# Performance work log

Measured on AMD Instinct MI355X. Metric: run time of the kernel, lower is better.

## Reference

```python
import jax, jax.numpy as jnp
import numpy as np

N_NODES = 100000
SIG_DIM = 64
N_ADJ = 1600000
N_QUERY = 262144


def setup_inputs() -> dict:
    key = jax.random.key(0)
    k1, k2, k3, k4, k5 = jax.random.split(key, 5)
    x = jax.random.normal(k1, (N_NODES, SIG_DIM), dtype=jnp.float32)
    x = x / jnp.linalg.norm(x, axis=1, keepdims=True)  # F.normalize(p=2, dim=1)
    node_weight = jax.random.uniform(k2, (N_NODES,), dtype=jnp.float32)
    edges = jax.random.randint(k3, (2, N_QUERY), 0, N_NODES)
    adj_row = jnp.sort(jax.random.randint(k4, (N_ADJ,), 0, N_NODES))
    adj_col = jax.random.randint(k5, (N_ADJ,), 0, N_NODES)
    return {
        "x": x,
        "node_weight": node_weight,
        "edges": edges,
        "adj_row": adj_row,
        "adj_col": adj_col,
        "num_nodes": N_NODES,
    }


def reference(x, node_weight, edges, adj_row, adj_col, num_nodes):
    # node signatures scaled by node weight
    xw = x * node_weight[:, None]                      # [N, D]

    seg = lambda vals: jax.ops.segment_sum(vals, adj_row, num_segments=num_nodes)

    # SpMM propagation: (A @ x)[i] = sum_{j in N(i)} x[j]
    one_hop = seg(xw[adj_col])                          # [N, D]
    deg = seg(jnp.ones_like(adj_row, dtype=xw.dtype))   # [N]
    two_iter = seg(one_hop[adj_col])                    # [N, D]

    # combine mode
    two_hop = two_iter - one_hop - xw
    deg2 = jnp.maximum(seg(deg[adj_col]) - deg - 1.0, 0.0)

    row, col = edges[0], edges[1]
    x_u_1 = one_hop[row]
    x_v_1 = one_hop[col]
    x_u_2 = two_hop[row]
    x_v_2 = two_hop[col]

    dot = lambda a, b: (a * b).sum(axis=-1)

    deg_u = deg[row]
    deg_v = deg[col]
    deg_u_2 = deg2[row]
    deg_v_2 = deg2[col]

    count_1_1 = dot(x_u_1, x_v_1)
    count_1_2 = dot(x_u_1, x_v_2)
    count_2_1 = dot(x_u_2, x_v_1)
    count_2_2 = dot(x_u_2, x_v_2)
    count_1_inf = deg_u + deg_v - 2 * count_1_1 - count_1_2 - count_2_1
    count_2_inf = deg_u_2 + deg_v_2 - 2 * count_2_2 - count_1_2 - count_2_1

    x_u_iter = two_iter[row]
    x_v_iter = two_iter[col]
    x_u = xw[row]
    x_v = xw[col]
    comb_count_1_2 = dot(x_u_1, x_v_iter)
    comb_count_2_1 = dot(x_u_iter, x_v_1)
    comb_count_2_2 = dot(x_u_iter - deg_u[:, None] * x_u,
                         x_v_iter - deg_v[:, None] * x_v)
    comb_count_self_1_2 = dot(x_u_1, x_u_iter)
    comb_count_self_2_1 = dot(x_v_1, x_v_iter)

    features = jnp.stack([
        count_1_1, count_1_2, count_2_1, count_2_2,
        count_1_inf, count_2_inf,
        comb_count_1_2, comb_count_2_1, comb_count_2_2,
        comb_count_self_1_2, comb_count_self_2_1,
        deg_u, deg_v, deg_u_2, deg_v_2,
    ], axis=1)                                          # [E, 15]
    return features
```

## Files before the change

kernel.cpp:

```cpp
#include <hip/hip_runtime.h>


#define D 64

typedef unsigned int uint32;
typedef _Float16 h2 __attribute__((ext_vector_type(2)));

union U32H2 { uint32 u; h2 h; };
__device__ __forceinline__ h2 u_as_h2(uint32 u) { U32H2 t; t.u = u; return t.h; }

__device__ __forceinline__ uint32 pack2(float a, float b) {
    uint32 ua = __float_as_uint(a);
    ua += 0x7fffu + ((ua >> 16) & 1u);
    uint32 ub = __float_as_uint(b);
    ub += 0x7fffu + ((ub >> 16) & 1u);
    return (ua >> 16) | (ub & 0xffff0000u);
}
__device__ __forceinline__ float lo2f(uint32 u) { return __uint_as_float(u << 16); }
__device__ __forceinline__ float hi2f(uint32 u) { return __uint_as_float(u & 0xffff0000u); }

__device__ __forceinline__ uint32 enc1(float v) {
    float a = fabsf(v);
    uint32 s = (__float_as_uint(v) >> 24) & 0x80u;
    if (a >= 448.f) return s | 0x7Eu;
    if (a < 0.015625f) {
        uint32 m = (uint32)rintf(a * 512.f);
        return (m > 7u) ? (s | 0x08u) : (s | m);
    }
    uint32 b = __float_as_uint(a);
    b += 0x7FFFFu + ((b >> 20) & 1u);
    uint32 m3 = (b >> 20) & 7u;
    int e4 = (int)(b >> 23) - 127 + 7;
    if (e4 > 15) return s | 0x7Eu;
    return s | ((uint32)e4 << 3) | m3;
}

__device__ __forceinline__ void dec8(uint32 u, uint32& pe, uint32& po) {
    uint32 se = (u << 8) & 0x80008000u;
    uint32 ue = u & 0x007f007fu;
    pe = ((ue << 7) + 0x08000800u) | se;
    uint32 so = u & 0x80008000u;
    uint32 uo = (u >> 8) & 0x007f007fu;
    po = ((uo << 7) + 0x08000800u) | so;
}

#define RED_GRP(v)  { v += __shfl_xor(v, 1, 64); v += __shfl_xor(v, 2, 64);  v += __shfl_xor(v, 4, 64);  }

__global__ void __launch_bounds__(256) prep_kernel(const float4* __restrict__ x,
                                                   const float* __restrict__ w,
                                                   uint2* __restrict__ xw,
                                                   const int* __restrict__ adj_row,
                                                   int* __restrict__ row_ptr,
                                                   int n8, int n, int nadj, int xw_blocks) {
    if ((int)blockIdx.x < xw_blocks) {
        int i = blockIdx.x * blockDim.x + threadIdx.x;
        if (i >= n8) return;
        float s = w[i >> 3] * 64.f;
        float4 a = x[i * 2], b = x[i * 2 + 1];
        uint32 w0 = enc1(a.x * s) | (enc1(a.z * s) << 8)
                  | (enc1(a.y * s) << 16) | (enc1(a.w * s) << 24);
        uint32 w1 = enc1(b.x * s) | (enc1(b.z * s) << 8)
                  | (enc1(b.y * s) << 16) | (enc1(b.w * s) << 24);
        xw[i] = make_uint2(w0, w1);
    } else {
        int i = (blockIdx.x - xw_blocks) * blockDim.x + threadIdx.x;
        if (i > n) return;
        int lo = 0, hi = nadj;
        while (lo < hi) {
            int mid = (lo + hi) >> 1;
            if (adj_row[mid] < i) lo = mid + 1; else hi = mid;
        }
        row_ptr[i] = lo;
    }
}

__global__ void __launch_bounds__(256) spmm1_kernel(const uint2* __restrict__ src,
                                                    const int* __restrict__ row_ptr,
                                                    const int* __restrict__ adj_col,
                                                    uint4* __restrict__ dst,
                                                    float* __restrict__ degout,
                                                    int n) {
    int lane = threadIdx.x & 63;
    int sub = lane & 7;
    int node = blockIdx.x * 32 + (threadIdx.x >> 6) * 8 + (lane >> 3);
    if (node >= n) return;
    int start = row_ptr[node], end = row_ptr[node + 1];
    int deg_n = end - start;
    h2 acc0 = u_as_h2(0u), acc1 = u_as_h2(0u), acc2 = u_as_h2(0u), acc3 = u_as_h2(0u);
    int gbase = lane & 56;
    const int* colp = adj_col + start;
    int base = 0;
    for (; base + 16 <= deg_n; base += 16) {
        int idx0 = colp[base + sub];
        int idx1 = colp[base + 8 + sub];
#pragma unroll
        for (int i = 0; i < 8; ++i) {
            int c0 = __shfl(idx0, gbase + i, 64);
            int c1 = __shfl(idx1, gbase + i, 64);
            uint2 q0 = src[(size_t)c0 * 8 + sub];
            uint2 q1 = src[(size_t)c1 * 8 + sub];
            uint32 pe, po;
            dec8(q0.x, pe, po);
            acc0 += u_as_h2(pe); acc1 += u_as_h2(po);
            dec8(q0.y, pe, po);
            acc2 += u_as_h2(pe); acc3 += u_as_h2(po);
            dec8(q1.x, pe, po);
            acc0 += u_as_h2(pe); acc1 += u_as_h2(po);
            dec8(q1.y, pe, po);
            acc2 += u_as_h2(pe); acc3 += u_as_h2(po);
        }
    }
    for (; base + 8 <= deg_n; base += 8) {
        int idx = colp[base + sub];
#pragma unroll
        for (int i = 0; i < 8; ++i) {
            int c = __shfl(idx, gbase + i, 64);
            uint2 qv = src[(size_t)c * 8 + sub];
            uint32 pe, po;
            dec8(qv.x, pe, po);
            acc0 += u_as_h2(pe); acc1 += u_as_h2(po);
            dec8(qv.y, pe, po);
            acc2 += u_as_h2(pe); acc3 += u_as_h2(po);
        }
    }
    if (base < deg_n) {
        int k = base + sub;
        int idx = (k < deg_n) ? colp[k] : 0;
#pragma unroll
        for (int i = 0; i < 8; ++i) {
            if (base + i < deg_n) {
                int c = __shfl(idx, gbase + i, 64);
                uint2 qv = src[(size_t)c * 8 + sub];
                uint32 pe, po;
                dec8(qv.x, pe, po);
                acc0 += u_as_h2(pe); acc1 += u_as_h2(po);
                dec8(qv.y, pe, po);
                acc2 += u_as_h2(pe); acc3 += u_as_h2(po);
            }
        }
    }
    uint4 o;
    o.x = pack2((float)acc0.x, (float)acc0.y);
    o.y = pack2((float)acc1.x, (float)acc1.y);
    o.z = pack2((float)acc2.x, (float)acc2.y);
    o.w = pack2((float)acc3.x, (float)acc3.y);
    dst[(size_t)node * 8 + sub] = o;
    if (sub == 0) degout[node] = (float)deg_n;
}

__global__ void __launch_bounds__(256) spmm2_kernel(const uint4* __restrict__ src,
                                                    const int* __restrict__ row_ptr,
                                                    const int* __restrict__ adj_col,
                                                    const float* __restrict__ degv,
                                                    uint4* __restrict__ dst,
                                                    float2* __restrict__ degpair,
                                                    int n) {
    int lane = threadIdx.x & 63;
    int sub = lane & 7;
    int node = blockIdx.x * 32 + (threadIdx.x >> 6) * 8 + (lane >> 3);
    if (node >= n) return;
    int start = row_ptr[node], end = row_ptr[node + 1];
    int deg_n = end - start;
    float a0 = 0.f, a1 = 0.f, a2 = 0.f, a3 = 0.f,
          a4 = 0.f, a5 = 0.f, a6 = 0.f, a7 = 0.f;
    float dsum = 0.f;
    int gbase = lane & 56;
    const int* colp = adj_col + start;

#define SPMM2_BLK(IDX)                                                 \
    {                                                                  \
        dsum += degv[IDX];                                             \
        _Pragma("unroll")                                              \
        for (int i = 0; i < 8; ++i) {                                  \
            int c = __shfl(IDX, gbase + i, 64);                        \
            uint4 qv = src[(size_t)c * 8 + sub];                       \
            a0 += lo2f(qv.x); a1 += hi2f(qv.x);                        \
            a2 += lo2f(qv.y); a3 += hi2f(qv.y);                        \
            a4 += lo2f(qv.z); a5 += hi2f(qv.z);                        \
            a6 += lo2f(qv.w); a7 += hi2f(qv.w);                        \
        }                                                              \
    }

    int nfull = deg_n >> 3;
    if (nfull > 0) {
        int idx = colp[sub];
        for (int b = 1; b < nfull; ++b) {
            int idxn = colp[b * 8 + sub];
            SPMM2_BLK(idx)
            idx = idxn;
        }
        SPMM2_BLK(idx)
    }
    int base = nfull * 8;
    if (base < deg_n) {
        int k = base + sub;
        bool kv = k < deg_n;
        int idx = kv ? colp[k] : 0;
        if (kv) dsum += degv[idx];
#pragma unroll
        for (int i = 0; i < 8; ++i) {
            if (base + i < deg_n) {
                int c = __shfl(idx, gbase + i, 64);
                uint4 qv = src[(size_t)c * 8 + sub];
                a0 += lo2f(qv.x); a1 += hi2f(qv.x);
                a2 += lo2f(qv.y); a3 += hi2f(qv.y);
                a4 += lo2f(qv.z); a5 += hi2f(qv.z);
                a6 += lo2f(qv.w); a7 += hi2f(qv.w);
            }
        }
    }
#undef SPMM2_BLK
    uint4 o;
    o.x = pack2(a0, a1); o.y = pack2(a2, a3);
    o.z = pack2(a4, a5); o.w = pack2(a6, a7);
    dst[(size_t)node * 8 + sub] = o;
    RED_GRP(dsum)
    if (sub == 0)
        degpair[node] = make_float2((float)deg_n,
                                    fmaxf(dsum - (float)deg_n - 1.0f, 0.0f));
}

__global__ void __launch_bounds__(256) edge_kernel(const int* __restrict__ edges,
                                                   const uint2* __restrict__ xw,
                                                   const uint4* __restrict__ h1,
                                                   const uint4* __restrict__ t2,
                                                   const float2* __restrict__ degpair,
                                                   float* __restrict__ out,
                                                   int E) {
    __shared__ float so[32 * 15];
    int t = blockIdx.x * blockDim.x + threadIdx.x;
    int q = t >> 3, sub = t & 7;
    bool valid = q < E;
    if (valid) {
        int u = edges[q], v = edges[E + q];
        uint2 pxu = xw[(size_t)u * 8 + sub], pxv = xw[(size_t)v * 8 + sub];
        uint4 phu = h1[(size_t)u * 8 + sub], phv = h1[(size_t)v * 8 + sub];
        uint4 ptu = t2[(size_t)u * 8 + sub], ptv = t2[(size_t)v * 8 + sub];
        float2 dpu = degpair[u], dpv = degpair[v];
        float du = dpu.x, du2 = dpu.y, dv = dpv.x, dv2 = dpv.y;

        float fxu[8], fxv[8], fhu[8], fhv[8], ftu[8], ftv[8];
        {
            uint32 pe, po;
            dec8(pxu.x, pe, po);
            h2 e = u_as_h2(pe), o_ = u_as_h2(po);
            fxu[0] = (float)e.x; fxu[1] = (float)e.y; fxu[2] = (float)o_.x; fxu[3] = (float)o_.y;
            dec8(pxu.y, pe, po);
            e = u_as_h2(pe); o_ = u_as_h2(po);
            fxu[4] = (float)e.x; fxu[5] = (float)e.y; fxu[6] = (float)o_.x; fxu[7] = (float)o_.y;
            dec8(pxv.x, pe, po);
            e = u_as_h2(pe); o_ = u_as_h2(po);
            fxv[0] = (float)e.x; fxv[1] = (float)e.y; fxv[2] = (float)o_.x; fxv[3] = (float)o_.y;
            dec8(pxv.y, pe, po);
            e = u_as_h2(pe); o_ = u_as_h2(po);
            fxv[4] = (float)e.x; fxv[5] = (float)e.y; fxv[6] = (float)o_.x; fxv[7] = (float)o_.y;
        }
        fhu[0]=lo2f(phu.x); fhu[1]=hi2f(phu.x); fhu[2]=lo2f(phu.y); fhu[3]=hi2f(phu.y);
        fhu[4]=lo2f(phu.z); fhu[5]=hi2f(phu.z); fhu[6]=lo2f(phu.w); fhu[7]=hi2f(phu.w);
        fhv[0]=lo2f(phv.x); fhv[1]=hi2f(phv.x); fhv[2]=lo2f(phv.y); fhv[3]=hi2f(phv.y);
        fhv[4]=lo2f(phv.z); fhv[5]=hi2f(phv.z); fhv[6]=lo2f(phv.w); fhv[7]=hi2f(phv.w);
        ftu[0]=lo2f(ptu.x); ftu[1]=hi2f(ptu.x); ftu[2]=lo2f(ptu.y); ftu[3]=hi2f(ptu.y);
        ftu[4]=lo2f(ptu.z); ftu[5]=hi2f(ptu.z); ftu[6]=lo2f(ptu.w); ftu[7]=hi2f(ptu.w);
        ftv[0]=lo2f(ptv.x); ftv[1]=hi2f(ptv.x); ftv[2]=lo2f(ptv.y); ftv[3]=hi2f(ptv.y);
        ftv[4]=lo2f(ptv.z); ftv[5]=hi2f(ptv.z); ftv[6]=lo2f(ptv.w); ftv[7]=hi2f(ptv.w);

        float c11 = 0.f, c12 = 0.f, c21 = 0.f, c22 = 0.f,
              cc12 = 0.f, cc21 = 0.f, cc22 = 0.f, cs12 = 0.f, cs21 = 0.f;
#pragma unroll
        for (int j = 0; j < 8; ++j) {
            float xu = fxu[j], xv = fxv[j];
            float hu = fhu[j], hv = fhv[j];
            float tu = ftu[j], tv = ftv[j];
            float h2u = tu - hu - xu, h2v = tv - hv - xv;
            float au = fmaf(-du, xu, tu), av = fmaf(-dv, xv, tv);
            c11  = fmaf(hu,  hv,  c11);
            c12  = fmaf(hu,  h2v, c12);
            c21  = fmaf(h2u, hv,  c21);
            c22  = fmaf(h2u, h2v, c22);
            cc12 = fmaf(hu,  tv,  cc12);
            cc21 = fmaf(tu,  hv,  cc21);
            cc22 = fmaf(au,  av,  cc22);
            cs12 = fmaf(hu,  tu,  cs12);
            cs21 = fmaf(hv,  tv,  cs21);
        }
        RED_GRP(c11) RED_GRP(c12) RED_GRP(c21) RED_GRP(c22)
        RED_GRP(cc12) RED_GRP(cc21) RED_GRP(cc22) RED_GRP(cs12) RED_GRP(cs21)

        if (sub == 0) {
            float* o = so + (threadIdx.x >> 3) * 15;
            o[0]  = c11;
            o[1]  = c12;
            o[2]  = c21;
            o[3]  = c22;
            o[4]  = du + dv - 2.f * c11 - c12 - c21;
            o[5]  = du2 + dv2 - 2.f * c22 - c12 - c21;
            o[6]  = cc12;
            o[7]  = cc21;
            o[8]  = cc22;
            o[9]  = cs12;
            o[10] = cs21;
            o[11] = du;
            o[12] = dv;
            o[13] = du2;
            o[14] = dv2;
        }
    }
    __syncthreads();
    int eb = blockIdx.x * 32;
    if (eb < E) {
        int nval = E - eb; if (nval > 32) nval = 32;
        int nflt = nval * 15;
        size_t obase = (size_t)eb * 15;
        for (int k = threadIdx.x; k < nflt; k += 256)
            out[obase + k] = so[k];
    }
}

extern "C" void kernel_launch(void* const* d_in, const int* in_sizes, int n_in,
                              void* d_out, int out_size, void* d_ws, size_t ws_size,
                              hipStream_t stream) {
    const float* x       = (const float*)d_in[0];
    const float* w       = (const float*)d_in[1];
    const int*   edges   = (const int*)d_in[2];
    const int*   adj_row = (const int*)d_in[3];
    const int*   adj_col = (const int*)d_in[4];

    const int N    = in_sizes[1];
    const int E    = in_sizes[2] / 2;
    const int NADJ = in_sizes[3];

    char* ws = (char*)d_ws;
    size_t off = 0;
    auto take = [&](size_t bytes) {
        void* p = ws + off;
        off = (off + bytes + 255) & ~(size_t)255;
        return p;
    };
    uint2*  xw      = (uint2*)take((size_t)N * 8 * sizeof(uint2));
    uint4*  one_hop = (uint4*)take((size_t)N * D * 2);
    uint4*  two_it  = (uint4*)take((size_t)N * D * 2);
    float*  deg     = (float*)take((size_t)N * sizeof(float));
    float2* degpair = (float2*)take((size_t)N * sizeof(float2));
    int*    row_ptr = (int*)take((size_t)(N + 1) * sizeof(int));
    (void)ws_size;

    float* out = (float*)d_out;

    {
        int n8 = N * 8;
        int xw_blocks = (n8 + 255) / 256;
        int rp_blocks = (N + 1 + 255) / 256;
        prep_kernel<<<xw_blocks + rp_blocks, 256, 0, stream>>>(
            (const float4*)x, w, xw, adj_row, row_ptr, n8, N, NADJ, xw_blocks);
    }
    spmm1_kernel<<<(N + 31) / 32, 256, 0, stream>>>(xw, row_ptr, adj_col, one_hop, deg, N);
    spmm2_kernel<<<(N + 31) / 32, 256, 0, stream>>>(one_hop, row_ptr, adj_col, deg,
                                                    two_it, degpair, N);
    edge_kernel<<<((size_t)E * 8 + 255) / 256, 256, 0, stream>>>(edges, xw, one_hop, two_it,
                                                                 degpair, out, E);
}
```

Measured before the change: 190.9 us.

## Fuse four kernels into one persistent cooperative kernel with grid syncs

Replaces the prep, spmm1, spmm2 and edge kernels with a single cooperative persistent kernel that uses grid-stride loops and separates the phases with grid.sync(). The aim is to remove per-kernel launch gaps and tail effects. In exchange it adds grid-wide barrier cost, is limited to occupancy-sized grids, and may run at lower occupancy because of the launch_bounds(256,4) register cap.

New measurement: 413.4 us. +116.6%, slower.

```diff
diff --git a/kernel.cpp b/kernel.cpp
--- a/kernel.cpp
+++ b/kernel.cpp
@@ -1,4 +1,7 @@
 #include <hip/hip_runtime.h>
+#include <hip/hip_cooperative_groups.h>
+
+namespace cg = cooperative_groups;
 
 
 #define D 64
@@ -46,91 +49,85 @@
 
 #define RED_GRP(v)  { v += __shfl_xor(v, 1, 64); v += __shfl_xor(v, 2, 64);  v += __shfl_xor(v, 4, 64);  }
 
-__global__ void __launch_bounds__(256) prep_kernel(const float4* __restrict__ x,
-                                                   const float* __restrict__ w,
-                                                   uint2* __restrict__ xw,
-                                                   const int* __restrict__ adj_row,
-                                                   int* __restrict__ row_ptr,
-                                                   int n8, int n, int nadj, int xw_blocks) {
-    if ((int)blockIdx.x < xw_blocks) {
-        int i = blockIdx.x * blockDim.x + threadIdx.x;
-        if (i >= n8) return;
-        float s = w[i >> 3] * 64.f;
-        float4 a = x[i * 2], b = x[i * 2 + 1];
-        uint32 w0 = enc1(a.x * s) | (enc1(a.z * s) << 8)
-                  | (enc1(a.y * s) << 16) | (enc1(a.w * s) << 24);
-        uint32 w1 = enc1(b.x * s) | (enc1(b.z * s) << 8)
-                  | (enc1(b.y * s) << 16) | (enc1(b.w * s) << 24);
-        xw[i] = make_uint2(w0, w1);
-    } else {
-        int i = (blockIdx.x - xw_blocks) * blockDim.x + threadIdx.x;
-        if (i > n) return;
-        int lo = 0, hi = nadj;
-        while (lo < hi) {
-            int mid = (lo + hi) >> 1;
-            if (adj_row[mid] < i) lo = mid + 1; else hi = mid;
-        }
-        row_ptr[i] = lo;
-    }
-}
-
-__global__ void __launch_bounds__(256) spmm1_kernel(const uint2* __restrict__ src,
-                                                    const int* __restrict__ row_ptr,
-                                                    const int* __restrict__ adj_col,
-                                                    uint4* __restrict__ dst,
-                                                    float* __restrict__ degout,
-                                                    int n) {
-    int lane = threadIdx.x & 63;
-    int sub = lane & 7;
-    int node = blockIdx.x * 32 + (threadIdx.x >> 6) * 8 + (lane >> 3);
-    if (node >= n) return;
-    int start = row_ptr[node], end = row_ptr[node + 1];
-    int deg_n = end - start;
-    h2 acc0 = u_as_h2(0u), acc1 = u_as_h2(0u), acc2 = u_as_h2(0u), acc3 = u_as_h2(0u);
-    int gbase = lane & 56;
-    const int* colp = adj_col + start;
-    int base = 0;
-    for (; base + 16 <= deg_n; base += 16) {
-        int idx0 = colp[base + sub];
-        int idx1 = colp[base + 8 + sub];
-#pragma unroll
-        for (int i = 0; i < 8; ++i) {
-            int c0 = __shfl(idx0, gbase + i, 64);
-            int c1 = __shfl(idx1, gbase + i, 64);
-            uint2 q0 = src[(size_t)c0 * 8 + sub];
-            uint2 q1 = src[(size_t)c1 * 8 + sub];
-            uint32 pe, po;
-            dec8(q0.x, pe, po);
-            acc0 += u_as_h2(pe); acc1 += u_as_h2(po);
-            dec8(q0.y, pe, po);
-            acc2 += u_as_h2(pe); acc3 += u_as_h2(po);
-            dec8(q1.x, pe, po);
-            acc0 += u_as_h2(pe); acc1 += u_as_h2(po);
-            dec8(q1.y, pe, po);
-            acc2 += u_as_h2(pe); acc3 += u_as_h2(po);
-        }
-    }
-    for (; base + 8 <= deg_n; base += 8) {
-        int idx = colp[base + sub];
-#pragma unroll
-        for (int i = 0; i < 8; ++i) {
-            int c = __shfl(idx, gbase + i, 64);
-            uint2 qv = src[(size_t)c * 8 + sub];
-            uint32 pe, po;
-            dec8(qv.x, pe, po);
-            acc0 += u_as_h2(pe); acc1 += u_as_h2(po);
-            dec8(qv.y, pe, po);
-            acc2 += u_as_h2(pe); acc3 += u_as_h2(po);
-        }
-    }
-    if (base < deg_n) {
-        int k = base + sub;
-        int idx = (k < deg_n) ? colp[k] : 0;
-#pragma unroll
-        for (int i = 0; i < 8; ++i) {
-            if (base + i < deg_n) {
+__global__ void __launch_bounds__(256, 4) fused_kernel(
+        const float4* __restrict__ x,
+        const float*  __restrict__ w,
+        const int*    __restrict__ edges,
+        const int*    __restrict__ adj_row,
+        const int*    __restrict__ adj_col,
+        uint2*  __restrict__ xw,
+        uint4*  __restrict__ one_hop,
+        uint4*  __restrict__ two_it,
+        float*  __restrict__ degv,
+        float2* __restrict__ degpair,
+        int*    __restrict__ row_ptr,
+        float*  __restrict__ out,
+        int n, int nadj, int E) {
+    cg::grid_group grid = cg::this_grid();
+    __shared__ float so[32 * 15];
+
+    const int tid = blockIdx.x * blockDim.x + threadIdx.x;
+    const int nthreads = gridDim.x * blockDim.x;
+    const int lane = threadIdx.x & 63;
+    const int sub = lane & 7;
+    const int gbase = lane & 56;
+
+    {
+        int n8 = n * 8;
+        for (int i = tid; i < n8; i += nthreads) {
+            float s = w[i >> 3] * 64.f;
+            float4 a = x[i * 2], b = x[i * 2 + 1];
+            uint32 w0 = enc1(a.x * s) | (enc1(a.z * s) << 8)
+                      | (enc1(a.y * s) << 16) | (enc1(a.w * s) << 24);
+            uint32 w1 = enc1(b.x * s) | (enc1(b.z * s) << 8)
+                      | (enc1(b.y * s) << 16) | (enc1(b.w * s) << 24);
+            xw[i] = make_uint2(w0, w1);
+        }
+        for (int i = tid; i <= n; i += nthreads) {
+            int lo = 0, hi = nadj;
+            while (lo < hi) {
+                int mid = (lo + hi) >> 1;
+                if (adj_row[mid] < i) lo = mid + 1; else hi = mid;
+            }
+            row_ptr[i] = lo;
+        }
+    }
+    grid.sync();
+
+    for (int nb = blockIdx.x * 32; nb < n; nb += gridDim.x * 32) {
+        int node = nb + (threadIdx.x >> 6) * 8 + (lane >> 3);
+        if (node >= n) continue;
+        int start = row_ptr[node], end = row_ptr[node + 1];
+        int deg_n = end - start;
+        h2 acc0 = u_as_h2(0u), acc1 = u_as_h2(0u), acc2 = u_as_h2(0u), acc3 = u_as_h2(0u);
+        const int* colp = adj_col + start;
+        int base = 0;
+        for (; base + 16 <= deg_n; base += 16) {
+            int idx0 = colp[base + sub];
+            int idx1 = colp[base + 8 + sub];
+#pragma unroll
+            for (int i = 0; i < 8; ++i) {
+                int c0 = __shfl(idx0, gbase + i, 64);
+                int c1 = __shfl(idx1, gbase + i, 64);
+                uint2 q0 = xw[(size_t)c0 * 8 + sub];
+                uint2 q1 = xw[(size_t)c1 * 8 + sub];
+                uint32 pe, po;
+                dec8(q0.x, pe, po);
+                acc0 += u_as_h2(pe); acc1 += u_as_h2(po);
+                dec8(q0.y, pe, po);
+                acc2 += u_as_h2(pe); acc3 += u_as_h2(po);
+                dec8(q1.x, pe, po);
+                acc0 += u_as_h2(pe); acc1 += u_as_h2(po);
+                dec8(q1.y, pe, po);
+                acc2 += u_as_h2(pe); acc3 += u_as_h2(po);
+            }
+        }
+        for (; base + 8 <= deg_n; base += 8) {
+            int idx = colp[base + sub];
+#pragma unroll
+            for (int i = 0; i < 8; ++i) {
                 int c = __shfl(idx, gbase + i, 64);
-                uint2 qv = src[(size_t)c * 8 + sub];
+                uint2 qv = xw[(size_t)c * 8 + sub];
                 uint32 pe, po;
                 dec8(qv.x, pe, po);
                 acc0 += u_as_h2(pe); acc1 += u_as_h2(po);
@@ -138,196 +135,194 @@
                 acc2 += u_as_h2(pe); acc3 += u_as_h2(po);
             }
         }
-    }
-    uint4 o;
-    o.x = pack2((float)acc0.x, (float)acc0.y);
-    o.y = pack2((float)acc1.x, (float)acc1.y);
-    o.z = pack2((float)acc2.x, (float)acc2.y);
-    o.w = pack2((float)acc3.x, (float)acc3.y);
-    dst[(size_t)node * 8 + sub] = o;
-    if (sub == 0) degout[node] = (float)deg_n;
-}
-
-__global__ void __launch_bounds__(256) spmm2_kernel(const uint4* __restrict__ src,
-                                                    const int* __restrict__ row_ptr,
-                                                    const int* __restrict__ adj_col,
-                                                    const float* __restrict__ degv,
-                                                    uint4* __restrict__ dst,
-                                                    float2* __restrict__ degpair,
-                                                    int n) {
-    int lane = threadIdx.x & 63;
-    int sub = lane & 7;
-    int node = blockIdx.x * 32 + (threadIdx.x >> 6) * 8 + (lane >> 3);
-    if (node >= n) return;
-    int start = row_ptr[node], end = row_ptr[node + 1];
-    int deg_n = end - start;
-    float a0 = 0.f, a1 = 0.f, a2 = 0.f, a3 = 0.f,
-          a4 = 0.f, a5 = 0.f, a6 = 0.f, a7 = 0.f;
-    float dsum = 0.f;
-    int gbase = lane & 56;
-    const int* colp = adj_col + start;
+        if (base < deg_n) {
+            int k = base + sub;
+            int idx = (k < deg_n) ? colp[k] : 0;
+#pragma unroll
+            for (int i = 0; i < 8; ++i) {
+                if (base + i < deg_n) {
+                    int c = __shfl(idx, gbase + i, 64);
+                    uint2 qv = xw[(size_t)c * 8 + sub];
+                    uint32 pe, po;
+                    dec8(qv.x, pe, po);
+                    acc0 += u_as_h2(pe); acc1 += u_as_h2(po);
+                    dec8(qv.y, pe, po);
+                    acc2 += u_as_h2(pe); acc3 += u_as_h2(po);
+                }
+            }
+        }
+        uint4 o;
+        o.x = pack2((float)acc0.x, (float)acc0.y);
+        o.y = pack2((float)acc1.x, (float)acc1.y);
+        o.z = pack2((float)acc2.x, (float)acc2.y);
+        o.w = pack2((float)acc3.x, (float)acc3.y);
+        one_hop[(size_t)node * 8 + sub] = o;
+        if (sub == 0) degv[node] = (float)deg_n;
+    }
+    grid.sync();
+
+    for (int nb = blockIdx.x * 32; nb < n; nb += gridDim.x * 32) {
+        int node = nb + (threadIdx.x >> 6) * 8 + (lane >> 3);
+        if (node >= n) continue;
+        int start = row_ptr[node], end = row_ptr[node + 1];
+        int deg_n = end - start;
+        float a0 = 0.f, a1 = 0.f, a2 = 0.f, a3 = 0.f,
+              a4 = 0.f, a5 = 0.f, a6 = 0.f, a7 = 0.f;
+        float dsum = 0.f;
+        const int* colp = adj_col + start;
 
 #define SPMM2_BLK(IDX)                                                 \
-    {                                                                  \
-        dsum += degv[IDX];                                             \
-        _Pragma("unroll")                                              \
-        for (int i = 0; i < 8; ++i) {                                  \
-            int c = __shfl(IDX, gbase + i, 64);                        \
-            uint4 qv = src[(size_t)c * 8 + sub];                       \
-            a0 += lo2f(qv.x); a1 += hi2f(qv.x);                        \
-            a2 += lo2f(qv.y); a3 += hi2f(qv.y);                        \
-            a4 += lo2f(qv.z); a5 += hi2f(qv.z);                        \
-            a6 += lo2f(qv.w); a7 += hi2f(qv.w);                        \
-        }                                                              \
-    }
-
-    int nfull = deg_n >> 3;
-    if (nfull > 0) {
-        int idx = colp[sub];
-        for (int b = 1; b < nfull; ++b) {
-            int idxn = colp[b * 8 + sub];
+        {                                                              \
+            dsum += degv[IDX];                                         \
+            _Pragma("unroll")                                          \
+            for (int i = 0; i < 8; ++i) {                              \
+                int c = __shfl(IDX, gbase + i, 64);                    \
+                uint4 qv = one_hop[(size_t)c * 8 + sub];               \
+                a0 += lo2f(qv.x); a1 += hi2f(qv.x);                    \
+                a2 += lo2f(qv.y); a3 += hi2f(qv.y);                    \
+                a4 += lo2f(qv.z); a5 += hi2f(qv.z);                    \
+                a6 += lo2f(qv.w); a7 += hi2f(qv.w);                    \
+            }                                                          \
+        }
+
+        int nfull = deg_n >> 3;
+        if (nfull > 0) {
+            int idx = colp[sub];
+            for (int b = 1; b < nfull; ++b) {
+                int idxn = colp[b * 8 + sub];
+                SPMM2_BLK(idx)
+                idx = idxn;
+            }
             SPMM2_BLK(idx)
-            idx = idxn;
-        }
-        SPMM2_BLK(idx)
-    }
-    int base = nfull * 8;
-    if (base < deg_n) {
-        int k = base + sub;
-        bool kv = k < deg_n;
-        int idx = kv ? colp[k] : 0;
-        if (kv) dsum += degv[idx];
-#pragma unroll
-        for (int i = 0; i < 8; ++i) {
-            if (base + i < deg_n) {
-                int c = __shfl(idx, gbase + i, 64);
-                uint4 qv = src[(size_t)c * 8 + sub];
-                a0 += lo2f(qv.x); a1 += hi2f(qv.x);
-                a2 += lo2f(qv.y); a3 += hi2f(qv.y);
-                a4 += lo2f(qv.z); a5 += hi2f(qv.z);
-                a6 += lo2f(qv.w); a7 += hi2f(qv.w);
-            }
-        }
-    }
+        }
+        int base = nfull * 8;
+        if (base < deg_n) {
+            int k = base + sub;
+            bool kv = k < deg_n;
+            int idx = kv ? colp[k] : 0;
+            if (kv) dsum += degv[idx];
+#pragma unroll
+            for (int i = 0; i < 8; ++i) {
+                if (base + i < deg_n) {
+                    int c = __shfl(idx, gbase + i, 64);
+                    uint4 qv = one_hop[(size_t)c * 8 + sub];
+                    a0 += lo2f(qv.x); a1 += hi2f(qv.x);
+                    a2 += lo2f(qv.y); a3 += hi2f(qv.y);
+                    a4 += lo2f(qv.z); a5 += hi2f(qv.z);
+                    a6 += lo2f(qv.w); a7 += hi2f(qv.w);
+                }
+            }
+        }
 #undef SPMM2_BLK
-    uint4 o;
-    o.x = pack2(a0, a1); o.y = pack2(a2, a3);
-    o.z = pack2(a4, a5); o.w = pack2(a6, a7);
-    dst[(size_t)node * 8 + sub] = o;
-    RED_GRP(dsum)
-    if (sub == 0)
-        degpair[node] = make_float2((float)deg_n,
-                                    fmaxf(dsum - (float)deg_n - 1.0f, 0.0f));
-}
-
-__global__ void __launch_bounds__(256) edge_kernel(const int* __restrict__ edges,
-                                                   const uint2* __restrict__ xw,
-                                                   const uint4* __restrict__ h1,
-                                                   const uint4* __restrict__ t2,
-                                                   const float2* __restrict__ degpair,
-                                                   float* __restrict__ out,
-                                                   int E) {
-    __shared__ float so[32 * 15];
-    int t = blockIdx.x * blockDim.x + threadIdx.x;
-    int q = t >> 3, sub = t & 7;
-    bool valid = q < E;
-    if (valid) {
-        int u = edges[q], v = edges[E + q];
-        uint2 pxu = xw[(size_t)u * 8 + sub], pxv = xw[(size_t)v * 8 + sub];
-        uint4 phu = h1[(size_t)u * 8 + sub], phv = h1[(size_t)v * 8 + sub];
-        uint4 ptu = t2[(size_t)u * 8 + sub], ptv = t2[(size_t)v * 8 + sub];
-        float2 dpu = degpair[u], dpv = degpair[v];
-        float du = dpu.x, du2 = dpu.y, dv = dpv.x, dv2 = dpv.y;
-
-        float fxu[8], fxv[8], fhu[8], fhv[8], ftu[8], ftv[8];
-        {
-            uint32 pe, po;
-            dec8(pxu.x, pe, po);
-            h2 e = u_as_h2(pe), o_ = u_as_h2(po);
-            fxu[0] = (float)e.x; fxu[1] = (float)e.y; fxu[2] = (float)o_.x; fxu[3] = (float)o_.y;
-            dec8(pxu.y, pe, po);
-            e = u_as_h2(pe); o_ = u_as_h2(po);
-            fxu[4] = (float)e.x; fxu[5] = (float)e.y; fxu[6] = (float)o_.x; fxu[7] = (float)o_.y;
-            dec8(pxv.x, pe, po);
-            e = u_as_h2(pe); o_ = u_as_h2(po);
-            fxv[0] = (float)e.x; fxv[1] = (float)e.y; fxv[2] = (float)o_.x; fxv[3] = (float)o_.y;
-            dec8(pxv.y, pe, po);
-            e = u_as_h2(pe); o_ = u_as_h2(po);
-            fxv[4] = (float)e.x; fxv[5] = (float)e.y; fxv[6] = (float)o_.x; fxv[7] = (float)o_.y;
-        }
-        fhu[0]=lo2f(phu.x); fhu[1]=hi2f(phu.x); fhu[2]=lo2f(phu.y); fhu[3]=hi2f(phu.y);
-        fhu[4]=lo2f(phu.z); fhu[5]=hi2f(phu.z); fhu[6]=lo2f(phu.w); fhu[7]=hi2f(phu.w);
-        fhv[0]=lo2f(phv.x); fhv[1]=hi2f(phv.x); fhv[2]=lo2f(phv.y); fhv[3]=hi2f(phv.y);
-        fhv[4]=lo2f(phv.z); fhv[5]=hi2f(phv.z); fhv[6]=lo2f(phv.w); fhv[7]=hi2f(phv.w);
-        ftu[0]=lo2f(ptu.x); ftu[1]=hi2f(ptu.x); ftu[2]=lo2f(ptu.y); ftu[3]=hi2f(ptu.y);
-        ftu[4]=lo2f(ptu.z); ftu[5]=hi2f(ptu.z); ftu[6]=lo2f(ptu.w); ftu[7]=hi2f(ptu.w);
-        ftv[0]=lo2f(ptv.x); ftv[1]=hi2f(ptv.x); ftv[2]=lo2f(ptv.y); ftv[3]=hi2f(ptv.y);
-        ftv[4]=lo2f(ptv.z); ftv[5]=hi2f(ptv.z); ftv[6]=lo2f(ptv.w); ftv[7]=hi2f(ptv.w);
-
-        float c11 = 0.f, c12 = 0.f, c21 = 0.f, c22 = 0.f,
-              cc12 = 0.f, cc21 = 0.f, cc22 = 0.f, cs12 = 0.f, cs21 = 0.f;
-#pragma unroll
-        for (int j = 0; j < 8; ++j) {
-            float xu = fxu[j], xv = fxv[j];
-            float hu = fhu[j], hv = fhv[j];
-            float tu = ftu[j], tv = ftv[j];
-            float h2u = tu - hu - xu, h2v = tv - hv - xv;
-            float au = fmaf(-du, xu, tu), av = fmaf(-dv, xv, tv);
-            c11  = fmaf(hu,  hv,  c11);
-            c12  = fmaf(hu,  h2v, c12);
-            c21  = fmaf(h2u, hv,  c21);
-            c22  = fmaf(h2u, h2v, c22);
-            cc12 = fmaf(hu,  tv,  cc12);
-            cc21 = fmaf(tu,  hv,  cc21);
-            cc22 = fmaf(au,  av,  cc22);
-            cs12 = fmaf(hu,  tu,  cs12);
-            cs21 = fmaf(hv,  tv,  cs21);
-        }
-        RED_GRP(c11) RED_GRP(c12) RED_GRP(c21) RED_GRP(c22)
-        RED_GRP(cc12) RED_GRP(cc21) RED_GRP(cc22) RED_GRP(cs12) RED_GRP(cs21)
-
-        if (sub == 0) {
-            float* o = so + (threadIdx.x >> 3) * 15;
-            o[0]  = c11;
-            o[1]  = c12;
-            o[2]  = c21;
-            o[3]  = c22;
-            o[4]  = du + dv - 2.f * c11 - c12 - c21;
-            o[5]  = du2 + dv2 - 2.f * c22 - c12 - c21;
-            o[6]  = cc12;
-            o[7]  = cc21;
-            o[8]  = cc22;
-            o[9]  = cs12;
-            o[10] = cs21;
-            o[11] = du;
-            o[12] = dv;
-            o[13] = du2;
-            o[14] = dv2;
-        }
-    }
-    __syncthreads();
-    int eb = blockIdx.x * 32;
-    if (eb < E) {
+        uint4 o;
+        o.x = pack2(a0, a1); o.y = pack2(a2, a3);
+        o.z = pack2(a4, a5); o.w = pack2(a6, a7);
+        two_it[(size_t)node * 8 + sub] = o;
+        RED_GRP(dsum)
+        if (sub == 0)
+            degpair[node] = make_float2((float)deg_n,
+                                        fmaxf(dsum - (float)deg_n - 1.0f, 0.0f));
+    }
+    grid.sync();
+
+    for (int eb = blockIdx.x * 32; eb < E; eb += gridDim.x * 32) {
+        int q = eb + (threadIdx.x >> 3);
+        if (q < E) {
+            int u = edges[q], v = edges[E + q];
+            uint2 pxu = xw[(size_t)u * 8 + sub], pxv = xw[(size_t)v * 8 + sub];
+            uint4 phu = one_hop[(size_t)u * 8 + sub], phv = one_hop[(size_t)v * 8 + sub];
+            uint4 ptu = two_it[(size_t)u * 8 + sub], ptv = two_it[(size_t)v * 8 + sub];
+            float2 dpu = degpair[u], dpv = degpair[v];
+            float du = dpu.x, du2 = dpu.y, dv = dpv.x, dv2 = dpv.y;
+
+            float fxu[8], fxv[8], fhu[8], fhv[8], ftu[8], ftv[8];
+            {
+                uint32 pe, po;
+                dec8(pxu.x, pe, po);
+                h2 e = u_as_h2(pe), o_ = u_as_h2(po);
+                fxu[0] = (float)e.x; fxu[1] = (float)e.y; fxu[2] = (float)o_.x; fxu[3] = (float)o_.y;
+                dec8(pxu.y, pe, po);
+                e = u_as_h2(pe); o_ = u_as_h2(po);
+                fxu[4] = (float)e.x; fxu[5] = (float)e.y; fxu[6] = (float)o_.x; fxu[7] = (float)o_.y;
+                dec8(pxv.x, pe, po);
+                e = u_as_h2(pe); o_ = u_as_h2(po);
+                fxv[0] = (float)e.x; fxv[1] = (float)e.y; fxv[2] = (float)o_.x; fxv[3] = (float)o_.y;
+                dec8(pxv.y, pe, po);
+                e = u_as_h2(pe); o_ = u_as_h2(po);
+                fxv[4] = (float)e.x; fxv[5] = (float)e.y; fxv[6] = (float)o_.x; fxv[7] = (float)o_.y;
+            }
+            fhu[0]=lo2f(phu.x); fhu[1]=hi2f(phu.x); fhu[2]=lo2f(phu.y); fhu[3]=hi2f(phu.y);
+            fhu[4]=lo2f(phu.z); fhu[5]=hi2f(phu.z); fhu[6]=lo2f(phu.w); fhu[7]=hi2f(phu.w);
+            fhv[0]=lo2f(phv.x); fhv[1]=hi2f(phv.x); fhv[2]=lo2f(phv.y); fhv[3]=hi2f(phv.y);
+            fhv[4]=lo2f(phv.z); fhv[5]=hi2f(phv.z); fhv[6]=lo2f(phv.w); fhv[7]=hi2f(phv.w);
+            ftu[0]=lo2f(ptu.x); ftu[1]=hi2f(ptu.x); ftu[2]=lo2f(ptu.y); ftu[3]=hi2f(ptu.y);
+            ftu[4]=lo2f(ptu.z); ftu[5]=hi2f(ptu.z); ftu[6]=lo2f(ptu.w); ftu[7]=hi2f(ptu.w);
+            ftv[0]=lo2f(ptv.x); ftv[1]=hi2f(ptv.x); ftv[2]=lo2f(ptv.y); ftv[3]=hi2f(ptv.y);
+            ftv[4]=lo2f(ptv.z); ftv[5]=hi2f(ptv.z); ftv[6]=lo2f(ptv.w); ftv[7]=hi2f(ptv.w);
+
+            float c11 = 0.f, c12 = 0.f, c21 = 0.f, c22 = 0.f,
+                  cc12 = 0.f, cc21 = 0.f, cc22 = 0.f, cs12 = 0.f, cs21 = 0.f;
+#pragma unroll
+            for (int j = 0; j < 8; ++j) {
+                float xu = fxu[j], xv = fxv[j];
+                float hu = fhu[j], hv = fhv[j];
+                float tu = ftu[j], tv = ftv[j];
+                float h2u = tu - hu - xu, h2v = tv - hv - xv;
+                float au = fmaf(-du, xu, tu), av = fmaf(-dv, xv, tv);
+                c11  = fmaf(hu,  hv,  c11);
+                c12  = fmaf(hu,  h2v, c12);
+                c21  = fmaf(h2u, hv,  c21);
+                c22  = fmaf(h2u, h2v, c22);
+                cc12 = fmaf(hu,  tv,  cc12);
+                cc21 = fmaf(tu,  hv,  cc21);
+                cc22 = fmaf(au,  av,  cc22);
+                cs12 = fmaf(hu,  tu,  cs12);
+                cs21 = fmaf(hv,  tv,  cs21);
+            }
+            RED_GRP(c11) RED_GRP(c12) RED_GRP(c21) RED_GRP(c22)
+            RED_GRP(cc12) RED_GRP(cc21) RED_GRP(cc22) RED_GRP(cs12) RED_GRP(cs21)
+
+            if (sub == 0) {
+                float* o = so + (threadIdx.x >> 3) * 15;
+                o[0]  = c11;
+                o[1]  = c12;
+                o[2]  = c21;
+                o[3]  = c22;
+                o[4]  = du + dv - 2.f * c11 - c12 - c21;
+                o[5]  = du2 + dv2 - 2.f * c22 - c12 - c21;
+                o[6]  = cc12;
+                o[7]  = cc21;
+                o[8]  = cc22;
+                o[9]  = cs12;
+                o[10] = cs21;
+                o[11] = du;
+                o[12] = dv;
+                o[13] = du2;
+                o[14] = dv2;
+            }
+        }
+        __syncthreads();
         int nval = E - eb; if (nval > 32) nval = 32;
         int nflt = nval * 15;
         size_t obase = (size_t)eb * 15;
         for (int k = threadIdx.x; k < nflt; k += 256)
             out[obase + k] = so[k];
+        __syncthreads();
     }
 }
 
 extern "C" void kernel_launch(void* const* d_in, const int* in_sizes, int n_in,
                               void* d_out, int out_size, void* d_ws, size_t ws_size,
                               hipStream_t stream) {
-    const float* x       = (const float*)d_in[0];
-    const float* w       = (const float*)d_in[1];
-    const int*   edges   = (const int*)d_in[2];
-    const int*   adj_row = (const int*)d_in[3];
-    const int*   adj_col = (const int*)d_in[4];
-
-    const int N    = in_sizes[1];
-    const int E    = in_sizes[2] / 2;
-    const int NADJ = in_sizes[3];
+    const float4* x     = (const float4*)d_in[0];
+    const float* w      = (const float*)d_in[1];
+    const int*   edges  = (const int*)d_in[2];
+    const int*   adj_row= (const int*)d_in[3];
+    const int*   adj_col= (const int*)d_in[4];
+
+    int N    = in_sizes[1];
+    int E    = in_sizes[2] / 2;
+    int NADJ = in_sizes[3];
 
     char* ws = (char*)d_ws;
     size_t off = 0;
@@ -346,16 +341,24 @@
 
     float* out = (float*)d_out;
 
-    {
-        int n8 = N * 8;
-        int xw_blocks = (n8 + 255) / 256;
-        int rp_blocks = (N + 1 + 255) / 256;
-        prep_kernel<<<xw_blocks + rp_blocks, 256, 0, stream>>>(
-            (const float4*)x, w, xw, adj_row, row_ptr, n8, N, NADJ, xw_blocks);
-    }
-    spmm1_kernel<<<(N + 31) / 32, 256, 0, stream>>>(xw, row_ptr, adj_col, one_hop, deg, N);
-    spmm2_kernel<<<(N + 31) / 32, 256, 0, stream>>>(one_hop, row_ptr, adj_col, deg,
-                                                    two_it, degpair, N);
-    edge_kernel<<<((size_t)E * 8 + 255) / 256, 256, 0, stream>>>(edges, xw, one_hop, two_it,
-                                                                 degpair, out, E);
-}
+    static int s_grid = 0;
+    if (s_grid == 0) {
+        int dev = 0;
+        hipGetDevice(&dev);
+        int cus = 0;
+        hipDeviceGetAttribute(&cus, hipDeviceAttributeMultiprocessorCount, dev);
+        if (cus < 1) cus = 256;
+        int bpc = 0;
+        hipOccupancyMaxActiveBlocksPerMultiprocessor(&bpc, fused_kernel, 256, 0);
+        if (bpc < 1) bpc = 1;
+        s_grid = bpc * cus;
+    }
+
+    void* args[] = {
+        (void*)&x, (void*)&w, (void*)&edges, (void*)&adj_row, (void*)&adj_col,
+        (void*)&xw, (void*)&one_hop, (void*)&two_it, (void*)&deg, (void*)&degpair,
+        (void*)&row_ptr, (void*)&out, (void*)&N, (void*)&NADJ, (void*)&E,
+    };
+    hipLaunchCooperativeKernel((const void*)fused_kernel, dim3(s_grid), dim3(256),
+                               args, 0, stream);
+}
```
